# Kernel tuning notes

Measured on AMD Instinct MI355X. Metric: run time of the kernel, lower is better.

The kernel has to match this reference:

```python
import jax, jax.numpy as jnp
import numpy as np

N_E = 16384
E_DIM = 64
GROUPS = 4
N_E_GROUP = N_E // GROUPS  # 4096
B, H, W = 16, 32, 32


def _l2norm(x):
    # matches F.normalize(p=2, dim=-1) with eps=1e-12
    n = jnp.linalg.norm(x, axis=-1, keepdims=True)
    return x / jnp.maximum(n, 1e-12)


def setup_inputs() -> dict:
    key = jax.random.key(0)
    k1, k2 = jax.random.split(key)
    z_groups = jax.random.normal(k1, (B, GROUPS * E_DIM, H, W), dtype=jnp.float32)
    emb = jax.random.uniform(k2, (N_E, E_DIM), minval=-1.0 / N_E, maxval=1.0 / N_E,
                             dtype=jnp.float32)
    emb = _l2norm(emb)  # module normalizes codebook at init when l2_norm=True
    return {"z_groups": z_groups, "embedding": emb}


def reference(z_groups, embedding):
    # Eval-mode forward (no EMA/random-restart buffer updates, losses are 0).
    b, c, h, w = z_groups.shape
    # split channels into groups: b (g*c) h w -> b h w g c
    z = z_groups.reshape(b, GROUPS, E_DIM, h, w).transpose(0, 3, 4, 1, 2)
    z = _l2norm(z)                                     # l2_norm=True path
    zf = z.reshape(-1, GROUPS, E_DIM)                  # [N, g, c]
    emb = _l2norm(embedding.reshape(GROUPS, N_E_GROUP, E_DIM))  # [g, k, c]

    # d = -|z|^2 - |e|^2 + 2 z.e  (negative squared distance), argmax = nearest
    d = (2.0 * jnp.einsum('ngc,gkc->ngk', zf, emb)
         - jnp.sum(zf * zf, axis=-1)[..., None]
         - jnp.sum(emb * emb, axis=-1)[None, :, :])    # [N, g, k]
    idx = jnp.argmax(d, axis=-1)                       # [N, g]

    zq = emb[jnp.arange(GROUPS)[None, :], idx]         # [N, g, c] gather
    zq = zf + jax.lax.stop_gradient(zq - zf)           # straight-through

    # b h w g c -> b (g*c) h w
    quant = zq.reshape(b, h, w, GROUPS, E_DIM).transpose(0, 3, 4, 1, 2)
    quant = quant.reshape(b, GROUPS * E_DIM, h, w)

    vq_loss = jnp.zeros((GROUPS,), jnp.float32)
    commit_loss = jnp.zeros((GROUPS,), jnp.float32)
    codebook_usage = jnp.zeros((GROUPS,), jnp.float32)

    # perplexity / min_encodings correspond to the last group (loop semantics)
    min_encodings = jax.nn.one_hot(idx[:, -1], N_E_GROUP, dtype=quant.dtype)
    avg_probs = jnp.mean(min_encodings, axis=0)
    perplexity = jnp.exp(-jnp.sum(avg_probs * jnp.log(avg_probs + 1e-10)))

    return (quant, vq_loss, commit_loss, codebook_usage,
            perplexity, min_encodings, idx)
```

## Files before the change

### kernel.cpp

```cpp
#include <hip/hip_runtime.h>
#include <hip/hip_bf16.h>
#include <math.h>

#define N_E      16384
#define E_DIM    64
#define GROUPS   4
#define N_E_G    4096
#define NQ       16384

#define OFF_QUANT   0L
#define OFF_VQLOSS  4194304L
#define OFF_PERP    4194316L
#define OFF_MINENC  4194317L
#define OFF_IDX     71303181L

#define WS_EN     0L
#define WS_EN2    1048576L
#define WS_ENHI   1064960L
#define WS_ZNR    1589248L
#define WS_ZHI    5783552L
#define WS_HIST   7880704L
#define WS_IDX3   7884800L

typedef float  float4v  __attribute__((ext_vector_type(4)));
typedef short  short8   __attribute__((ext_vector_type(8)));

static __device__ __forceinline__ ushort f2bf(float x) {
    union { __hip_bfloat16 h; ushort u; } cv; cv.h = __float2bfloat16(x);
    return cv.u;
}

__global__ void norm_all_kernel(const float* __restrict__ emb,
                                const float* __restrict__ z,
                                float* __restrict__ en, float* __restrict__ en2,
                                ushort* __restrict__ ehi,
                                float* __restrict__ znr, ushort* __restrict__ zhi,
                                int* __restrict__ hist) {
    __shared__ float tile[64 * 65];
    __shared__ float rden[64];
    const int t = threadIdx.x;

    if (blockIdx.x == 4096 + 1024) {
        for (int i = t; i < N_E_G; i += 256) hist[i] = 0;
        return;
    }

    if (blockIdx.x < 4096) {
        int gid  = blockIdx.x * 256 + t;
        int code = gid >> 6;
        int k    = t & 63;
        float x = emb[code * 64 + k];
        float ss = x * x;
        #pragma unroll
        for (int off = 32; off; off >>= 1) ss += __shfl_xor(ss, off, 64);
        float v = x / fmaxf(sqrtf(ss), 1e-12f);
        en[code * 64 + k]  = v;
        ehi[code * 64 + k] = f2bf(v);
        float s2 = v * v;
        #pragma unroll
        for (int off = 32; off; off >>= 1) s2 += __shfl_xor(s2, off, 64);
        if (k == 0) en2[code] = s2;
        return;
    }

    int bx2 = blockIdx.x - 4096;
    int g   = bx2 >> 8;
    int n0  = (bx2 & 255) * 64;
    int b   = n0 >> 10, hw0 = n0 & 1023;
    const float* src = z + (size_t)b * 262144 + (size_t)g * 65536 + hw0;

    for (int i = t; i < 4096; i += 256) {
        int d = i >> 6, nl = i & 63;
        tile[d * 65 + nl] = src[(size_t)d * 1024 + nl];
    }
    __syncthreads();

    if (t < 64) {
        float ss = 0.f;
        for (int d = 0; d < 64; ++d) {
            float x = tile[d * 65 + t];
            ss = fmaf(x, x, ss);
        }
        rden[t] = fmaxf(sqrtf(ss), 1e-12f);
    }
    __syncthreads();

    for (int i = t; i < 4096; i += 256) {
        int q = i >> 6, d = i & 63;
        float v = tile[d * 65 + q] / rden[q];
        size_t o = ((size_t)g * NQ + n0 + q) * 64 + d;
        znr[o] = v;
        zhi[o] = f2bf(v);
    }
}

#define CAP  64
#define TAU  0.017f
__global__ __launch_bounds__(256, 4)
void vq_cand_kernel(const ushort* __restrict__ zhi, const ushort* __restrict__ ehi,
                    const float* __restrict__ znr, const float* __restrict__ en,
                    const float* __restrict__ en2, float* __restrict__ out,
                    int* __restrict__ hist, int* __restrict__ idx3) {
    __shared__ int    cnt[64];
    __shared__ ushort cand[64 * CAP];
    __shared__ int    bks[64];

    const int g  = blockIdx.y;
    const int q0 = blockIdx.x * 64;
    const int t  = threadIdx.x;
    const int wave = t >> 6, lane = t & 63;
    const int l15 = lane & 15, quad = lane >> 4;
    const int qhalf = wave & 1, chalf = wave >> 1;

    const int sliceId = g * 256 + blockIdx.x;
    float4v* fill4 = (float4v*)(out + OFF_VQLOSS) + (size_t)sliceId * 16384;
    const float4v z4 = {0.f, 0.f, 0.f, 0.f};

    if (t < 64) cnt[t] = 0;

    short8 bfrag[2][2];
    #pragma unroll
    for (int u = 0; u < 2; ++u)
        #pragma unroll
        for (int ks = 0; ks < 2; ++ks)
            bfrag[u][ks] = *(const short8*)(zhi +
                ((size_t)g * NQ + q0 + qhalf * 32 + u * 16 + l15) * 64
                + ks * 32 + quad * 8);
    __syncthreads();

    const ushort* abase = ehi + (size_t)g * N_E_G * 64
                        + (size_t)(chalf * 64 + l15) * 64 + quad * 8;

    float Mrun[2];
    Mrun[0] = -3.4e38f; Mrun[1] = -3.4e38f;

    for (int tile = 0; tile < 32; ++tile) {
        short8 af[4][2];
        {
            const ushort* p = abase + (size_t)(tile * 128) * 64;
            #pragma unroll
            for (int cs = 0; cs < 4; ++cs)
                #pragma unroll
                for (int ks = 0; ks < 2; ++ks)
                    af[cs][ks] = *(const short8*)(p + (size_t)(cs * 16) * 64 + ks * 32);
        }
        fill4[(size_t)(tile * 2 + 0) * 256 + t] = z4;
        fill4[(size_t)(tile * 2 + 1) * 256 + t] = z4;

        float4v acc[4][2];
        #pragma unroll
        for (int cs = 0; cs < 4; ++cs)
            #pragma unroll
            for (int u = 0; u < 2; ++u) {
                float4v zz = {0.f, 0.f, 0.f, 0.f};
                float4v tmp = __builtin_amdgcn_mfma_f32_16x16x32_bf16(
                                  af[cs][0], bfrag[u][0], zz, 0, 0, 0);
                acc[cs][u] = __builtin_amdgcn_mfma_f32_16x16x32_bf16(
                                  af[cs][1], bfrag[u][1], tmp, 0, 0, 0);
            }

        const int j0 = tile * 128;
        #pragma unroll
        for (int u = 0; u < 2; ++u) {
            float m = acc[0][u][0];
            #pragma unroll
            for (int cs = 0; cs < 4; ++cs)
                #pragma unroll
                for (int r = 0; r < 4; ++r) m = fmaxf(m, acc[cs][u][r]);
            float m2 = fmaxf(m, __shfl_xor(m, 16, 64));
            float m4 = fmaxf(m2, __shfl_xor(m2, 32, 64));
            Mrun[u] = fmaxf(Mrun[u], m4);
            float thr = Mrun[u] - TAU;
            if (m >= thr) {
                int ql = qhalf * 32 + u * 16 + l15;
                #pragma unroll
                for (int cs = 0; cs < 4; ++cs)
                    #pragma unroll
                    for (int r = 0; r < 4; ++r)
                        if (acc[cs][u][r] >= thr) {
                            int cidx = j0 + chalf * 64 + cs * 16 + quad * 4 + r;
                            int slot = atomicAdd(&cnt[ql], 1);
                            if (slot < CAP) cand[ql * CAP + slot] = (ushort)cidx;
                        }
            }
        }
    }

    if (sliceId == 0 && t < 13) out[OFF_VQLOSS + 67108864L + t] = 0.f;
    __syncthreads();

    if (t < 64) {
        int q = q0 + t;
        float za[64];
        const float4v* zp = (const float4v*)(znr + ((size_t)g * NQ + q) * 64);
        #pragma unroll
        for (int i = 0; i < 16; ++i) {
            float4v v = zp[i];
            za[i*4+0] = v[0]; za[i*4+1] = v[1]; za[i*4+2] = v[2]; za[i*4+3] = v[3];
        }
        int nc = cnt[t]; if (nc > CAP) nc = CAP;
        float best = -3.4e38f; int bk = 0x7fffffff;
        for (int s = 0; s < nc; ++s) {
            int c = cand[t * CAP + s];
            const float* ev = en + ((size_t)g * N_E_G + c) * 64;
            float a = 0.f;
            #pragma unroll
            for (int k = 0; k < 64; ++k) a = fmaf(za[k], ev[k], a);
            float d = 2.f * a - en2[g * N_E_G + c];
            if (d > best || (d == best && c < bk)) { best = d; bk = c; }
        }
        if (bk == 0x7fffffff) bk = 0;
        bks[t] = bk;
        out[OFF_IDX + (size_t)q * 4 + g] = (float)bk;
        if (g == 3) {
            idx3[q] = bk;
            atomicAdd(&hist[bk], 1);
        }
    }
    __syncthreads();

    for (int i = t; i < 64 * 64; i += 256) {
        int d = i >> 6, m = i & 63;
        int n = q0 + m, b = n >> 10, hw = n & 1023;
        out[OFF_QUANT + (size_t)b * 262144 + (size_t)(g * 64 + d) * 1024 + hw] =
            en[((size_t)g * N_E_G + bks[m]) * 64 + d];
    }
}

__global__ void finalize_kernel(const int* __restrict__ idx3,
                                const int* __restrict__ hist,
                                float* __restrict__ out) {
    if (blockIdx.x < 64) {
        int r = blockIdx.x * 256 + threadIdx.x;
        out[OFF_MINENC + (size_t)r * N_E_G + idx3[r]] = 1.0f;
        return;
    }
    __shared__ float s[256];
    int t = threadIdx.x;
    float acc = 0.f;
    for (int k = t; k < N_E_G; k += 256) {
        float p = (float)hist[k] * (1.0f / 16384.0f);
        acc += p * logf(p + 1e-10f);
    }
    s[t] = acc;
    __syncthreads();
    for (int o = 128; o; o >>= 1) {
        if (t < o) s[t] += s[t + o];
        __syncthreads();
    }
    if (t == 0) out[OFF_PERP] = expf(-s[0]);
}

extern "C" void kernel_launch(void* const* d_in, const int* in_sizes, int n_in,
                              void* d_out, int out_size, void* d_ws, size_t ws_size,
                              hipStream_t stream) {
    const float* z_groups = (const float*)d_in[0];
    const float* emb      = (const float*)d_in[1];
    float* out = (float*)d_out;
    float* ws  = (float*)d_ws;

    float*  en   = ws + WS_EN;
    float*  en2  = ws + WS_EN2;
    ushort* ehi  = (ushort*)(ws + WS_ENHI);
    float*  znr  = ws + WS_ZNR;
    ushort* zhi  = (ushort*)(ws + WS_ZHI);
    int*    hist = (int*)(ws + WS_HIST);
    int*    idx3 = (int*)(ws + WS_IDX3);

    norm_all_kernel<<<4096 + 1024 + 1, 256, 0, stream>>>(
        emb, z_groups, en, en2, ehi, znr, zhi, hist);

    vq_cand_kernel<<<dim3(256, GROUPS), 256, 0, stream>>>(
        zhi, ehi, znr, en, en2, out, hist, idx3);

    finalize_kernel<<<65, 256, 0, stream>>>(idx3, hist, out);
}
```

Before: 447.1 us.

## Fuse z normalization into candidate kernel and double queries per block

Moves the z transpose and L2 normalization from the prep kernel into the main VQ kernel, which now loads raw z into a shared tile and builds bf16 MFMA fragments and fp32 rescoring vectors from it. This drops the znr/zhi workspace round trip through global memory. Each block now handles 128 queries with 512 threads, halving how often the codebook is read across blocks. The cost is a larger shared-memory footprint, fewer blocks, and strided shared reads while building the fragments.

After: 436.0 us. 2.5% less time.

```diff
diff --git a/kernel.cpp b/kernel.cpp
--- a/kernel.cpp
+++ b/kernel.cpp
@@ -17,10 +17,8 @@
 #define WS_EN     0L
 #define WS_EN2    1048576L
 #define WS_ENHI   1064960L
-#define WS_ZNR    1589248L
-#define WS_ZHI    5783552L
-#define WS_HIST   7880704L
-#define WS_IDX3   7884800L
+#define WS_HIST   1589248L
+#define WS_IDX3   1593344L
 
 typedef float  float4v  __attribute__((ext_vector_type(4)));
 typedef short  short8   __attribute__((ext_vector_type(8)));
@@ -30,106 +28,95 @@
     return cv.u;
 }
 
-__global__ void norm_all_kernel(const float* __restrict__ emb,
-                                const float* __restrict__ z,
+__global__ void norm_emb_kernel(const float* __restrict__ emb,
                                 float* __restrict__ en, float* __restrict__ en2,
-                                ushort* __restrict__ ehi,
-                                float* __restrict__ znr, ushort* __restrict__ zhi,
-                                int* __restrict__ hist) {
-    __shared__ float tile[64 * 65];
-    __shared__ float rden[64];
+                                ushort* __restrict__ ehi, int* __restrict__ hist) {
     const int t = threadIdx.x;
-
-    if (blockIdx.x == 4096 + 1024) {
+    if (blockIdx.x == 4096) {
         for (int i = t; i < N_E_G; i += 256) hist[i] = 0;
         return;
     }
-
-    if (blockIdx.x < 4096) {
-        int gid  = blockIdx.x * 256 + t;
-        int code = gid >> 6;
-        int k    = t & 63;
-        float x = emb[code * 64 + k];
-        float ss = x * x;
-        #pragma unroll
-        for (int off = 32; off; off >>= 1) ss += __shfl_xor(ss, off, 64);
-        float v = x / fmaxf(sqrtf(ss), 1e-12f);
-        en[code * 64 + k]  = v;
-        ehi[code * 64 + k] = f2bf(v);
-        float s2 = v * v;
-        #pragma unroll
-        for (int off = 32; off; off >>= 1) s2 += __shfl_xor(s2, off, 64);
-        if (k == 0) en2[code] = s2;
-        return;
-    }
-
-    int bx2 = blockIdx.x - 4096;
-    int g   = bx2 >> 8;
-    int n0  = (bx2 & 255) * 64;
-    int b   = n0 >> 10, hw0 = n0 & 1023;
-    const float* src = z + (size_t)b * 262144 + (size_t)g * 65536 + hw0;
-
-    for (int i = t; i < 4096; i += 256) {
-        int d = i >> 6, nl = i & 63;
-        tile[d * 65 + nl] = src[(size_t)d * 1024 + nl];
-    }
-    __syncthreads();
-
-    if (t < 64) {
-        float ss = 0.f;
-        for (int d = 0; d < 64; ++d) {
-            float x = tile[d * 65 + t];
-            ss = fmaf(x, x, ss);
-        }
-        rden[t] = fmaxf(sqrtf(ss), 1e-12f);
-    }
-    __syncthreads();
-
-    for (int i = t; i < 4096; i += 256) {
-        int q = i >> 6, d = i & 63;
-        float v = tile[d * 65 + q] / rden[q];
-        size_t o = ((size_t)g * NQ + n0 + q) * 64 + d;
-        znr[o] = v;
-        zhi[o] = f2bf(v);
-    }
+    int gid  = blockIdx.x * 256 + t;
+    int code = gid >> 6;
+    int k    = t & 63;
+    float x = emb[code * 64 + k];
+    float ss = x * x;
+    #pragma unroll
+    for (int off = 32; off; off >>= 1) ss += __shfl_xor(ss, off, 64);
+    float v = x / fmaxf(sqrtf(ss), 1e-12f);
+    en[code * 64 + k]  = v;
+    ehi[code * 64 + k] = f2bf(v);
+    float s2 = v * v;
+    #pragma unroll
+    for (int off = 32; off; off >>= 1) s2 += __shfl_xor(s2, off, 64);
+    if (k == 0) en2[code] = s2;
 }
 
 #define CAP  64
 #define TAU  0.017f
-__global__ __launch_bounds__(256, 4)
-void vq_cand_kernel(const ushort* __restrict__ zhi, const ushort* __restrict__ ehi,
-                    const float* __restrict__ znr, const float* __restrict__ en,
-                    const float* __restrict__ en2, float* __restrict__ out,
+__global__ __launch_bounds__(512, 4)
+void vq_cand_kernel(const float* __restrict__ z, const ushort* __restrict__ ehi,
+                    const float* __restrict__ en, const float* __restrict__ en2,
+                    float* __restrict__ out,
                     int* __restrict__ hist, int* __restrict__ idx3) {
-    __shared__ int    cnt[64];
-    __shared__ ushort cand[64 * CAP];
-    __shared__ int    bks[64];
+    __shared__ float  ztile[64][129];
+    __shared__ float  rden[128];
+    __shared__ int    cnt[128];
+    __shared__ ushort cand[128 * CAP];
+    __shared__ int    bks[128];
 
     const int g  = blockIdx.y;
-    const int q0 = blockIdx.x * 64;
+    const int q0 = blockIdx.x * 128;
     const int t  = threadIdx.x;
     const int wave = t >> 6, lane = t & 63;
     const int l15 = lane & 15, quad = lane >> 4;
-    const int qhalf = wave & 1, chalf = wave >> 1;
-
-    const int sliceId = g * 256 + blockIdx.x;
-    float4v* fill4 = (float4v*)(out + OFF_VQLOSS) + (size_t)sliceId * 16384;
+    const int qh = wave & 3;
+    const int cq = wave >> 2;
+
+    const int sliceId = g * 128 + blockIdx.x;
+    float4v* fill4 = (float4v*)(out + OFF_VQLOSS) + (size_t)sliceId * 32768;
     const float4v z4 = {0.f, 0.f, 0.f, 0.f};
 
-    if (t < 64) cnt[t] = 0;
+    {
+        int b = q0 >> 10, hw0 = q0 & 1023;
+        const float* zsrc = z + (size_t)b * 262144 + (size_t)g * 65536 + hw0;
+        for (int i = t; i < 64 * 128; i += 512) {
+            int d = i >> 7, q = i & 127;
+            ztile[d][q] = zsrc[(size_t)d * 1024 + q];
+        }
+    }
+    if (t < 128) cnt[t] = 0;
+    __syncthreads();
+
+    if (t < 128) {
+        float ss = 0.f;
+        for (int d = 0; d < 64; ++d) {
+            float x = ztile[d][t];
+            ss = fmaf(x, x, ss);
+        }
+        rden[t] = fmaxf(sqrtf(ss), 1e-12f);
+    }
+    __syncthreads();
 
     short8 bfrag[2][2];
     #pragma unroll
-    for (int u = 0; u < 2; ++u)
-        #pragma unroll
-        for (int ks = 0; ks < 2; ++ks)
-            bfrag[u][ks] = *(const short8*)(zhi +
-                ((size_t)g * NQ + q0 + qhalf * 32 + u * 16 + l15) * 64
-                + ks * 32 + quad * 8);
-    __syncthreads();
+    for (int u = 0; u < 2; ++u) {
+        int q = qh * 32 + u * 16 + l15;
+        float den = rden[q];
+        #pragma unroll
+        for (int ks = 0; ks < 2; ++ks) {
+            short8 f;
+            #pragma unroll
+            for (int j = 0; j < 8; ++j) {
+                int k = ks * 32 + quad * 8 + j;
+                f[j] = (short)f2bf(ztile[k][q] / den);
+            }
+            bfrag[u][ks] = f;
+        }
+    }
 
     const ushort* abase = ehi + (size_t)g * N_E_G * 64
-                        + (size_t)(chalf * 64 + l15) * 64 + quad * 8;
+                        + (size_t)(cq * 64 + l15) * 64 + quad * 8;
 
     float Mrun[2];
     Mrun[0] = -3.4e38f; Mrun[1] = -3.4e38f;
@@ -144,8 +131,8 @@
                 for (int ks = 0; ks < 2; ++ks)
                     af[cs][ks] = *(const short8*)(p + (size_t)(cs * 16) * 64 + ks * 32);
         }
-        fill4[(size_t)(tile * 2 + 0) * 256 + t] = z4;
-        fill4[(size_t)(tile * 2 + 1) * 256 + t] = z4;
+        fill4[(size_t)(tile * 2 + 0) * 512 + t] = z4;
+        fill4[(size_t)(tile * 2 + 1) * 512 + t] = z4;
 
         float4v acc[4][2];
         #pragma unroll
@@ -172,13 +159,13 @@
             Mrun[u] = fmaxf(Mrun[u], m4);
             float thr = Mrun[u] - TAU;
             if (m >= thr) {
-                int ql = qhalf * 32 + u * 16 + l15;
+                int ql = qh * 32 + u * 16 + l15;
                 #pragma unroll
                 for (int cs = 0; cs < 4; ++cs)
                     #pragma unroll
                     for (int r = 0; r < 4; ++r)
                         if (acc[cs][u][r] >= thr) {
-                            int cidx = j0 + chalf * 64 + cs * 16 + quad * 4 + r;
+                            int cidx = j0 + cq * 64 + cs * 16 + quad * 4 + r;
                             int slot = atomicAdd(&cnt[ql], 1);
                             if (slot < CAP) cand[ql * CAP + slot] = (ushort)cidx;
                         }
@@ -189,15 +176,12 @@
     if (sliceId == 0 && t < 13) out[OFF_VQLOSS + 67108864L + t] = 0.f;
     __syncthreads();
 
-    if (t < 64) {
+    if (t < 128) {
         int q = q0 + t;
+        float den = rden[t];
         float za[64];
-        const float4v* zp = (const float4v*)(znr + ((size_t)g * NQ + q) * 64);
-        #pragma unroll
-        for (int i = 0; i < 16; ++i) {
-            float4v v = zp[i];
-            za[i*4+0] = v[0]; za[i*4+1] = v[1]; za[i*4+2] = v[2]; za[i*4+3] = v[3];
-        }
+        #pragma unroll
+        for (int k = 0; k < 64; ++k) za[k] = ztile[k][t] / den;
         int nc = cnt[t]; if (nc > CAP) nc = CAP;
         float best = -3.4e38f; int bk = 0x7fffffff;
         for (int s = 0; s < nc; ++s) {
@@ -219,8 +203,8 @@
     }
     __syncthreads();
 
-    for (int i = t; i < 64 * 64; i += 256) {
-        int d = i >> 6, m = i & 63;
+    for (int i = t; i < 128 * 64; i += 512) {
+        int d = i >> 7, m = i & 127;
         int n = q0 + m, b = n >> 10, hw = n & 1023;
         out[OFF_QUANT + (size_t)b * 262144 + (size_t)(g * 64 + d) * 1024 + hw] =
             en[((size_t)g * N_E_G + bks[m]) * 64 + d];
@@ -262,16 +246,13 @@
     float*  en   = ws + WS_EN;
     float*  en2  = ws + WS_EN2;
     ushort* ehi  = (ushort*)(ws + WS_ENHI);
-    float*  znr  = ws + WS_ZNR;
-    ushort* zhi  = (ushort*)(ws + WS_ZHI);
     int*    hist = (int*)(ws + WS_HIST);
     int*    idx3 = (int*)(ws + WS_IDX3);
 
-    norm_all_kernel<<<4096 + 1024 + 1, 256, 0, stream>>>(
-        emb, z_groups, en, en2, ehi, znr, zhi, hist);
-
-    vq_cand_kernel<<<dim3(256, GROUPS), 256, 0, stream>>>(
-        zhi, ehi, znr, en, en2, out, hist, idx3);
+    norm_emb_kernel<<<4097, 256, 0, stream>>>(emb, en, en2, ehi, hist);
+
+    vq_cand_kernel<<<dim3(NQ / 128, GROUPS), 512, 0, stream>>>(
+        z_groups, ehi, en, en2, out, hist, idx3);
 
     finalize_kernel<<<65, 256, 0, stream>>>(idx3, hist, out);
 }
```
